# Kernel tuning notes

Hardware: AMD Instinct MI355X
Metric: run time of the kernel (lower is better)

## Reference

```python
import jax, jax.numpy as jnp
import numpy as np

ALPHA = 0.2  # LeakyReLU negative slope


def setup_inputs() -> dict:
    key = jax.random.key(0)
    k1, k2, k3, k4 = jax.random.split(key, 4)
    N, F_in, F_out = 8192, 512, 64
    x = jax.random.normal(k1, (N, F_in), dtype=jnp.float32)
    adj = jax.random.uniform(k2, (N, N), dtype=jnp.float32)
    W = jax.random.normal(k3, (F_in, F_out), dtype=jnp.float32) * 0.05
    a = jax.random.normal(k4, (2 * F_out, 1), dtype=jnp.float32) * 0.05
    return {"x": x, "adj": adj, "W": W, "a": a}


def reference(x, adj, W, a):
    F_out = W.shape[1]
    h = x @ W                                   # [N, F_out]
    # Additive attention decomposed: score[i,j] = h[i]·a1 + h[j]·a2
    # (equivalent to concat([h_i, h_j]) @ a, without the N×N×2F blowup)
    a1 = a[:F_out, 0]                           # [F_out]
    a2 = a[F_out:, 0]                           # [F_out]
    e = jax.nn.leaky_relu(h @ a1[:, None] + (h @ a2)[None, :], ALPHA)  # [N, N]
    attention = jax.nn.softmax(e * adj, axis=1)  # elementwise mult, as in source
    # dropout skipped (eval / training=False -> identity)
    h_prime = attention @ h                      # [N, F_out]
    return jax.nn.elu(h_prime)                   # concat=True branch
```

## Files before the change

kernel.cpp:

```cpp
#include <hip/hip_runtime.h>

#define ALPHA 0.2f

typedef __attribute__((ext_vector_type(8))) short short8v;
typedef __attribute__((ext_vector_type(4))) float f32x4;

__device__ __forceinline__ unsigned cvt_pk_bf16(float a, float b) {
  unsigned d;
  asm("v_cvt_pk_bf16_f32 %0, %1, %2" : "=v"(d) : "v"(a), "v"(b));
  return d;
}

#define GLOAD_LDS16(gp, lp)                                                   \
  __builtin_amdgcn_global_load_lds(                                           \
      (const __attribute__((address_space(1))) unsigned int*)(gp),            \
      (__attribute__((address_space(3))) unsigned int*)(lp), 16, 0, 0)

__global__ __launch_bounds__(256) void k1_proj(
    const float* __restrict__ x, const float* __restrict__ W,
    const float* __restrict__ avec,
    short* __restrict__ hT, float* __restrict__ s1, float* __restrict__ s2,
    float* __restrict__ num) {
  __shared__ float xl[32 * 132];
  __shared__ float Wl[128 * 64];
  const int t   = threadIdx.x;
  const int rb  = blockIdx.x;
  const int row = t >> 3;
  const int fg  = t & 7;

  {
    float4 z = {0.f, 0.f, 0.f, 0.f};
    *(float4*)(num + rb * 2048 + t * 8)     = z;
    *(float4*)(num + rb * 2048 + t * 8 + 4) = z;
  }

  float acc[8];
#pragma unroll
  for (int e = 0; e < 8; e++) acc[e] = 0.f;

  for (int kc = 0; kc < 4; kc++) {
#pragma unroll
    for (int u = 0; u < 4; u++) {
      int lin = t + u * 256;
      int r = lin >> 5, c4 = lin & 31;
      float4 v = *(const float4*)(x + (size_t)(rb * 32 + r) * 512 + kc * 128 + c4 * 4);
      *(float4*)(xl + r * 132 + c4 * 4) = v;
    }
#pragma unroll
    for (int u = 0; u < 8; u++) {
      int lin = t + u * 256;
      int r = lin >> 4, c4 = lin & 15;
      float4 v = *(const float4*)(W + (size_t)(kc * 128 + r) * 64 + c4 * 4);
      *(float4*)(Wl + r * 64 + c4 * 4) = v;
    }
    __syncthreads();
#pragma unroll 8
    for (int k = 0; k < 128; k++) {
      float xv = xl[row * 132 + k];
      float4 w0 = *(const float4*)(Wl + k * 64 + fg * 8);
      float4 w1 = *(const float4*)(Wl + k * 64 + fg * 8 + 4);
      acc[0] = fmaf(xv, w0.x, acc[0]); acc[1] = fmaf(xv, w0.y, acc[1]);
      acc[2] = fmaf(xv, w0.z, acc[2]); acc[3] = fmaf(xv, w0.w, acc[3]);
      acc[4] = fmaf(xv, w1.x, acc[4]); acc[5] = fmaf(xv, w1.y, acc[5]);
      acc[6] = fmaf(xv, w1.z, acc[6]); acc[7] = fmaf(xv, w1.w, acc[7]);
    }
    __syncthreads();
  }

  float p1 = 0.f, p2 = 0.f;
#pragma unroll
  for (int e = 0; e < 8; e++) {
    p1 = fmaf(acc[e], avec[fg * 8 + e], p1);
    p2 = fmaf(acc[e], avec[64 + fg * 8 + e], p2);
  }
  p1 += __shfl_xor(p1, 1, 64); p1 += __shfl_xor(p1, 2, 64); p1 += __shfl_xor(p1, 4, 64);
  p2 += __shfl_xor(p2, 1, 64); p2 += __shfl_xor(p2, 2, 64); p2 += __shfl_xor(p2, 4, 64);
  const int gi = rb * 32 + row;
  if (fg == 0) { s1[gi] = p1; s2[gi] = p2; }
#pragma unroll
  for (int e = 0; e < 8; e++) {
    union { float f; unsigned u; } v; v.f = acc[e];
    unsigned rr = v.u + 0x7fffu + ((v.u >> 16) & 1u);
    hT[(size_t)(fg * 8 + e) * 8192 + gi] = (short)(rr >> 16);
  }
}

__global__ __launch_bounds__(256, 3) void k2_attn(
    const float* __restrict__ adj, const short* __restrict__ hT,
    const float* __restrict__ s1, const float* __restrict__ s2,
    float* __restrict__ num, float* __restrict__ den) {
  __shared__ short hP[16384];
  __shared__ short Pl[8192];
  const int t    = threadIdx.x;
  const int wvi  = t >> 6;
  const int l    = t & 63;
  const int lq   = l >> 4;
  const int lr   = l & 15;
  const int rb   = blockIdx.x & 127;
  const int ks   = blockIdx.x >> 7;
  const int r0   = rb << 6;
  const int j0   = ks << 8;

  float s1own = s1[r0 + wvi * 16 + lr];
#pragma unroll
  for (int r = 0; r < 8; r++) {
    const int d    = r * 4096 + t * 16;
    const int frow = d >> 9;
    const int lcb  = (d & 511) ^ ((frow & 7) << 4);
    GLOAD_LDS16(hT + (size_t)frow * 8192 + j0 + (lcb >> 1), (char*)hP + d);
  }
  float4 s2A4 = *(const float4*)(s2 + j0 + l * 4);

  __syncthreads();
  __builtin_amdgcn_sched_barrier(0);

  const float* ar = adj + (size_t)(r0 + wvi * 16) * 8192 + j0 + l * 4;
  float4 A0,A1,A2,A3,A4,A5,A6,A7,A8,A9,A10,A11,A12,A13,A14,A15;
  A0  = *(const float4*)(ar);
  A1  = *(const float4*)(ar + 1 * 8192);
  A2  = *(const float4*)(ar + 2 * 8192);
  A3  = *(const float4*)(ar + 3 * 8192);
  A4  = *(const float4*)(ar + 4 * 8192);
  A5  = *(const float4*)(ar + 5 * 8192);
  A6  = *(const float4*)(ar + 6 * 8192);
  A7  = *(const float4*)(ar + 7 * 8192);
  A8  = *(const float4*)(ar + 8 * 8192);
  A9  = *(const float4*)(ar + 9 * 8192);
  A10 = *(const float4*)(ar + 10 * 8192);
  A11 = *(const float4*)(ar + 11 * 8192);
  A12 = *(const float4*)(ar + 12 * 8192);
  A13 = *(const float4*)(ar + 13 * 8192);
  A14 = *(const float4*)(ar + 14 * 8192);
  A15 = *(const float4*)(ar + 15 * 8192);

  float s1r[16];
#pragma unroll
  for (int i = 0; i < 16; i++)
    s1r[i] = __int_as_float(
        __builtin_amdgcn_readfirstlane(__float_as_int(__shfl(s1own, i, 64))));

  float denom_p[16];
#pragma unroll
  for (int i = 0; i < 16; i++) denom_p[i] = 0.f;
  f32x4 acc[4];
#pragma unroll
  for (int fb = 0; fb < 4; fb++) acc[fb] = (f32x4){0.f, 0.f, 0.f, 0.f};

  char* Pw = (char*)Pl + wvi * 4096;
  unsigned pk0[16], pk1[16];

#define EXPROW4(I, AV, S2V) do {                                              \
    float z0 = s1r[I] + S2V.x; z0 = fmaxf(z0, ALPHA * z0) * AV.x;             \
    float z1 = s1r[I] + S2V.y; z1 = fmaxf(z1, ALPHA * z1) * AV.y;             \
    float z2 = s1r[I] + S2V.z; z2 = fmaxf(z2, ALPHA * z2) * AV.z;             \
    float z3 = s1r[I] + S2V.w; z3 = fmaxf(z3, ALPHA * z3) * AV.w;             \
    float w0 = __expf(z0), w1 = __expf(z1), w2 = __expf(z2), w3 = __expf(z3); \
    denom_p[I] += (w0 + w1) + (w2 + w3);                                      \
    pk0[I] = cvt_pk_bf16(w0, w1); pk1[I] = cvt_pk_bf16(w2, w3);               \
  } while (0)

#define PWRITE(HALF) do {                                                     \
    if ((l >> 5) == (HALF)) {                                                 \
      const int cb = (l & 31) * 8;                                            \
      _Pragma("unroll")                                                       \
      for (int i2 = 0; i2 < 16; i2++) {                                       \
        uint2 pv; pv.x = pk0[i2]; pv.y = pk1[i2];                             \
        *(uint2*)(Pw + (((i2 << 8) + cb) ^ ((i2 & 7) << 4))) = pv;            \
      }                                                                       \
    }                                                                         \
  } while (0)

#define MFMACHUNK(CL) do {                                                    \
    __builtin_amdgcn_s_setprio(1);                                            \
    _Pragma("unroll")                                                         \
    for (int kk = 0; kk < 4; kk++) {                                          \
      const int ab = ((lr << 8) + (kk << 6) + (lq << 4)) ^ ((lr & 7) << 4);   \
      const short8v au = *(const short8v*)(Pw + ab);                          \
      _Pragma("unroll")                                                       \
      for (int fb = 0; fb < 4; fb++) {                                        \
        const int fr = fb * 16 + lr;                                          \
        const int bb = ((fr << 9) + ((CL) << 8) + (kk << 6) + (lq << 4))      \
                       ^ ((fr & 7) << 4);                                     \
        const short8v bu = *(const short8v*)((char*)hP + bb);                 \
        acc[fb] = __builtin_amdgcn_mfma_f32_16x16x32_bf16(au, bu,             \
                                                          acc[fb], 0, 0, 0); \
      }                                                                       \
    }                                                                         \
    __builtin_amdgcn_s_setprio(0);                                            \
  } while (0)

  EXPROW4(0, A0, s2A4);   EXPROW4(1, A1, s2A4);   EXPROW4(2, A2, s2A4);
  EXPROW4(3, A3, s2A4);   EXPROW4(4, A4, s2A4);   EXPROW4(5, A5, s2A4);
  EXPROW4(6, A6, s2A4);   EXPROW4(7, A7, s2A4);   EXPROW4(8, A8, s2A4);
  EXPROW4(9, A9, s2A4);   EXPROW4(10, A10, s2A4); EXPROW4(11, A11, s2A4);
  EXPROW4(12, A12, s2A4); EXPROW4(13, A13, s2A4); EXPROW4(14, A14, s2A4);
  EXPROW4(15, A15, s2A4);
  PWRITE(0); MFMACHUNK(0);
  PWRITE(1); MFMACHUNK(1);

#undef EXPROW4
#undef PWRITE
#undef MFMACHUNK

#pragma unroll
  for (int i = 0; i < 16; i++) {
    float d = denom_p[i];
    d += __shfl_xor(d, 1, 64); d += __shfl_xor(d, 2, 64);
    d += __shfl_xor(d, 4, 64); d += __shfl_xor(d, 8, 64);
    d += __shfl_xor(d, 16, 64); d += __shfl_xor(d, 32, 64);
    if (l == 0) den[(size_t)ks * 8192 + r0 + wvi * 16 + i] = d;
  }
#pragma unroll
  for (int fb = 0; fb < 4; fb++)
#pragma unroll
    for (int r = 0; r < 4; r++)
      atomicAdd(&num[(size_t)(r0 + wvi * 16 + lq * 4 + r) * 64 + fb * 16 + lr],
                acc[fb][r]);
}

__global__ __launch_bounds__(256) void k3_norm(
    const float* __restrict__ num, const float* __restrict__ den,
    float* __restrict__ out) {
  const int idx = blockIdx.x * 256 + threadIdx.x;
  const int row = idx >> 6;
  float d = 0.f;
#pragma unroll
  for (int ksi = 0; ksi < 32; ksi++) d += den[ksi * 8192 + row];
  float v = num[idx] / d;
  out[idx] = v > 0.f ? v : (__expf(v) - 1.f);
}

extern "C" void kernel_launch(void* const* d_in, const int* in_sizes, int n_in,
                              void* d_out, int out_size, void* d_ws, size_t ws_size,
                              hipStream_t stream) {
  const float* x   = (const float*)d_in[0];
  const float* adj = (const float*)d_in[1];
  const float* W   = (const float*)d_in[2];
  const float* av  = (const float*)d_in[3];
  float* out = (float*)d_out;
  char* ws = (char*)d_ws;

  short* hT  = (short*)ws;
  float* s1  = (float*)(ws + (1 << 20));
  float* s2  = (float*)(ws + (1 << 20) + 32768);
  float* num = (float*)(ws + (1 << 20) + 65536);
  float* den = num + 524288u;

  hipLaunchKernelGGL(k1_proj, dim3(256), dim3(256), 0, stream,
                     x, W, av, hT, s1, s2, num);
  hipLaunchKernelGGL(k2_attn, dim3(4096), dim3(256), 0, stream,
                     adj, hT, s1, s2, num, den);
  hipLaunchKernelGGL(k3_norm, dim3(2048), dim3(256), 0, stream, num, den, out);
}
```

Before: 100.8 us.

## Widen attention tile to 1024 columns with 512-thread blocks and 8 rows per wave

The attention kernel now handles 1024 key columns per block instead of 256, using 8 waves that each own 8 rows. Each block stages a 128KB hT tile in LDS and loops over four 256-column groups. This cuts the split-K factor from 32 to 8, so there are fewer atomic adds to num and fewer partial denominators to sum. Because each MFMA expects 16 rows, half of the A operand is fed from a zeroed LDS buffer, which wastes half the MFMA throughput. The larger LDS footprint also lowers occupancy.

```diff
diff --git a/kernel.cpp b/kernel.cpp
--- a/kernel.cpp
+++ b/kernel.cpp
@@ -85,69 +85,71 @@
   }
 }
 
-__global__ __launch_bounds__(256, 3) void k2_attn(
+__global__ __launch_bounds__(512, 2) void k2_attn(
     const float* __restrict__ adj, const short* __restrict__ hT,
     const float* __restrict__ s1, const float* __restrict__ s2,
     float* __restrict__ num, float* __restrict__ den) {
-  __shared__ short hP[16384];
-  __shared__ short Pl[8192];
-  const int t    = threadIdx.x;
-  const int wvi  = t >> 6;
-  const int l    = t & 63;
-  const int lq   = l >> 4;
-  const int lr   = l & 15;
-  const int rb   = blockIdx.x & 127;
-  const int ks   = blockIdx.x >> 7;
-  const int r0   = rb << 6;
-  const int j0   = ks << 8;
-
-  float s1own = s1[r0 + wvi * 16 + lr];
-#pragma unroll
-  for (int r = 0; r < 8; r++) {
-    const int d    = r * 4096 + t * 16;
-    const int frow = d >> 9;
-    const int lcb  = (d & 511) ^ ((frow & 7) << 4);
+  __shared__ short hP[65536];
+  __shared__ short Pl[9216];
+  const int t   = threadIdx.x;
+  const int wv  = t >> 6;
+  const int l   = t & 63;
+  const int lq  = l >> 4;
+  const int lr  = l & 15;
+  const int rb  = blockIdx.x & 127;
+  const int ks  = blockIdx.x >> 7;
+  const int r0  = rb << 6;
+  const int j0  = ks << 10;
+
+  if (t < 128) {
+    short8v z = {0, 0, 0, 0, 0, 0, 0, 0};
+    *(short8v*)(Pl + 8192 + t * 8) = z;
+  }
+
+  float s1own = s1[r0 + wv * 8 + (l & 7)];
+
+#pragma unroll
+  for (int r = 0; r < 16; r++) {
+    const int d    = r * 8192 + t * 16;
+    const int frow = d >> 11;
+    const int lcb  = (d & 2047) ^ ((frow & 7) << 4);
     GLOAD_LDS16(hT + (size_t)frow * 8192 + j0 + (lcb >> 1), (char*)hP + d);
   }
-  float4 s2A4 = *(const float4*)(s2 + j0 + l * 4);
 
   __syncthreads();
   __builtin_amdgcn_sched_barrier(0);
 
-  const float* ar = adj + (size_t)(r0 + wvi * 16) * 8192 + j0 + l * 4;
-  float4 A0,A1,A2,A3,A4,A5,A6,A7,A8,A9,A10,A11,A12,A13,A14,A15;
-  A0  = *(const float4*)(ar);
-  A1  = *(const float4*)(ar + 1 * 8192);
-  A2  = *(const float4*)(ar + 2 * 8192);
-  A3  = *(const float4*)(ar + 3 * 8192);
-  A4  = *(const float4*)(ar + 4 * 8192);
-  A5  = *(const float4*)(ar + 5 * 8192);
-  A6  = *(const float4*)(ar + 6 * 8192);
-  A7  = *(const float4*)(ar + 7 * 8192);
-  A8  = *(const float4*)(ar + 8 * 8192);
-  A9  = *(const float4*)(ar + 9 * 8192);
-  A10 = *(const float4*)(ar + 10 * 8192);
-  A11 = *(const float4*)(ar + 11 * 8192);
-  A12 = *(const float4*)(ar + 12 * 8192);
-  A13 = *(const float4*)(ar + 13 * 8192);
-  A14 = *(const float4*)(ar + 14 * 8192);
-  A15 = *(const float4*)(ar + 15 * 8192);
-
-  float s1r[16];
-#pragma unroll
-  for (int i = 0; i < 16; i++)
-    s1r[i] = __int_as_float(
-        __builtin_amdgcn_readfirstlane(__float_as_int(__shfl(s1own, i, 64))));
-
-  float denom_p[16];
-#pragma unroll
-  for (int i = 0; i < 16; i++) denom_p[i] = 0.f;
+  const float* ar = adj + (size_t)(r0 + wv * 8) * 8192 + j0 + l * 4;
+  float4 A0_0,A0_1,A0_2,A0_3, A1_0,A1_1,A1_2,A1_3;
+  float4 A2_0,A2_1,A2_2,A2_3, A3_0,A3_1,A3_2,A3_3;
+  float4 A4_0,A4_1,A4_2,A4_3, A5_0,A5_1,A5_2,A5_3;
+  float4 A6_0,A6_1,A6_2,A6_3, A7_0,A7_1,A7_2,A7_3;
+#define LDROW(R) do { const float* p__ = ar + (R) * 8192;                     \
+    A##R##_0 = *(const float4*)(p__);        A##R##_1 = *(const float4*)(p__ + 256); \
+    A##R##_2 = *(const float4*)(p__ + 512);  A##R##_3 = *(const float4*)(p__ + 768); \
+  } while (0)
+  LDROW(0); LDROW(1); LDROW(2); LDROW(3);
+  LDROW(4); LDROW(5); LDROW(6); LDROW(7);
+#undef LDROW
+  float4 s2g0 = *(const float4*)(s2 + j0 + l * 4);
+  float4 s2g1 = *(const float4*)(s2 + j0 + 256 + l * 4);
+  float4 s2g2 = *(const float4*)(s2 + j0 + 512 + l * 4);
+  float4 s2g3 = *(const float4*)(s2 + j0 + 768 + l * 4);
+
+  float s1r[8];
+#pragma unroll
+  for (int i = 0; i < 8; i++) s1r[i] = __shfl(s1own, i, 64);
+
+  float denom_p[8];
+#pragma unroll
+  for (int i = 0; i < 8; i++) denom_p[i] = 0.f;
   f32x4 acc[4];
 #pragma unroll
   for (int fb = 0; fb < 4; fb++) acc[fb] = (f32x4){0.f, 0.f, 0.f, 0.f};
 
-  char* Pw = (char*)Pl + wvi * 4096;
-  unsigned pk0[16], pk1[16];
+  char* Pw = (char*)Pl + wv * 2048;
+  const char* Zb = (char*)Pl + 16384;
+  unsigned pk0[8], pk1[8];
 
 #define EXPROW4(I, AV, S2V) do {                                              \
     float z0 = s1r[I] + S2V.x; z0 = fmaxf(z0, ALPHA * z0) * AV.x;             \
@@ -163,7 +165,7 @@
     if ((l >> 5) == (HALF)) {                                                 \
       const int cb = (l & 31) * 8;                                            \
       _Pragma("unroll")                                                       \
-      for (int i2 = 0; i2 < 16; i2++) {                                       \
+      for (int i2 = 0; i2 < 8; i2++) {                                        \
         uint2 pv; pv.x = pk0[i2]; pv.y = pk1[i2];                             \
         *(uint2*)(Pw + (((i2 << 8) + cb) ^ ((i2 & 7) << 4))) = pv;            \
       }                                                                       \
@@ -174,12 +176,13 @@
     __builtin_amdgcn_s_setprio(1);                                            \
     _Pragma("unroll")                                                         \
     for (int kk = 0; kk < 4; kk++) {                                          \
-      const int ab = ((lr << 8) + (kk << 6) + (lq << 4)) ^ ((lr & 7) << 4);   \
-      const short8v au = *(const short8v*)(Pw + ab);                          \
+      const int abo = ((lr << 8) + (kk << 6) + (lq << 4)) ^ ((lr & 7) << 4);  \
+      const char* ap = (lr < 8) ? (Pw + abo) : Zb;                            \
+      const short8v au = *(const short8v*)ap;                                 \
       _Pragma("unroll")                                                       \
       for (int fb = 0; fb < 4; fb++) {                                        \
         const int fr = fb * 16 + lr;                                          \
-        const int bb = ((fr << 9) + ((CL) << 8) + (kk << 6) + (lq << 4))      \
+        const int bb = ((fr << 11) + ((CL) << 8) + (kk << 6) + (lq << 4))     \
                        ^ ((fr & 7) << 4);                                     \
         const short8v bu = *(const short8v*)((char*)hP + bb);                 \
         acc[fb] = __builtin_amdgcn_mfma_f32_16x16x32_bf16(au, bu,             \
@@ -189,33 +192,41 @@
     __builtin_amdgcn_s_setprio(0);                                            \
   } while (0)
 
-  EXPROW4(0, A0, s2A4);   EXPROW4(1, A1, s2A4);   EXPROW4(2, A2, s2A4);
-  EXPROW4(3, A3, s2A4);   EXPROW4(4, A4, s2A4);   EXPROW4(5, A5, s2A4);
-  EXPROW4(6, A6, s2A4);   EXPROW4(7, A7, s2A4);   EXPROW4(8, A8, s2A4);
-  EXPROW4(9, A9, s2A4);   EXPROW4(10, A10, s2A4); EXPROW4(11, A11, s2A4);
-  EXPROW4(12, A12, s2A4); EXPROW4(13, A13, s2A4); EXPROW4(14, A14, s2A4);
-  EXPROW4(15, A15, s2A4);
-  PWRITE(0); MFMACHUNK(0);
-  PWRITE(1); MFMACHUNK(1);
+#define GROUP(G) do {                                                         \
+    EXPROW4(0, A0_##G, s2g##G); EXPROW4(1, A1_##G, s2g##G);                   \
+    EXPROW4(2, A2_##G, s2g##G); EXPROW4(3, A3_##G, s2g##G);                   \
+    EXPROW4(4, A4_##G, s2g##G); EXPROW4(5, A5_##G, s2g##G);                   \
+    EXPROW4(6, A6_##G, s2g##G); EXPROW4(7, A7_##G, s2g##G);                   \
+    PWRITE(0); MFMACHUNK(2 * G);                                              \
+    PWRITE(1); MFMACHUNK(2 * G + 1);                                          \
+  } while (0)
+
+  GROUP(0);
+  GROUP(1);
+  GROUP(2);
+  GROUP(3);
 
 #undef EXPROW4
 #undef PWRITE
 #undef MFMACHUNK
-
-#pragma unroll
-  for (int i = 0; i < 16; i++) {
+#undef GROUP
+
+#pragma unroll
+  for (int i = 0; i < 8; i++) {
     float d = denom_p[i];
     d += __shfl_xor(d, 1, 64); d += __shfl_xor(d, 2, 64);
     d += __shfl_xor(d, 4, 64); d += __shfl_xor(d, 8, 64);
     d += __shfl_xor(d, 16, 64); d += __shfl_xor(d, 32, 64);
-    if (l == 0) den[(size_t)ks * 8192 + r0 + wvi * 16 + i] = d;
-  }
-#pragma unroll
-  for (int fb = 0; fb < 4; fb++)
-#pragma unroll
-    for (int r = 0; r < 4; r++)
-      atomicAdd(&num[(size_t)(r0 + wvi * 16 + lq * 4 + r) * 64 + fb * 16 + lr],
-                acc[fb][r]);
+    if (l == 0) den[(size_t)ks * 8192 + r0 + wv * 8 + i] = d;
+  }
+  if (lq < 2) {
+#pragma unroll
+    for (int fb = 0; fb < 4; fb++)
+#pragma unroll
+      for (int r = 0; r < 4; r++)
+        atomicAdd(&num[(size_t)(r0 + wv * 8 + lq * 4 + r) * 64 + fb * 16 + lr],
+                  acc[fb][r]);
+  }
 }
 
 __global__ __launch_bounds__(256) void k3_norm(
@@ -225,7 +236,7 @@
   const int row = idx >> 6;
   float d = 0.f;
 #pragma unroll
-  for (int ksi = 0; ksi < 32; ksi++) d += den[ksi * 8192 + row];
+  for (int ksi = 0; ksi < 8; ksi++) d += den[ksi * 8192 + row];
   float v = num[idx] / d;
   out[idx] = v > 0.f ? v : (__expf(v) - 1.f);
 }
@@ -248,7 +259,7 @@
 
   hipLaunchKernelGGL(k1_proj, dim3(256), dim3(256), 0, stream,
                      x, W, av, hT, s1, s2, num);
-  hipLaunchKernelGGL(k2_attn, dim3(4096), dim3(256), 0, stream,
+  hipLaunchKernelGGL(k2_attn, dim3(1024), dim3(512), 0, stream,
                      adj, hT, s1, s2, num, den);
   hipLaunchKernelGGL(k3_norm, dim3(2048), dim3(256), 0, stream, num, den, out);
 }
```

After: 101.9 us. Within noise of the previous version (+1.1%).
